# Optimization experiments

Hardware: AMD Instinct MI355X
Metric: run time of the kernel (lower is better)

## Reference

```python
import jax, jax.numpy as jnp
import numpy as np

N, D_IN, H, OUT, L = 6144, 512, 512, 256, 3
EPS = 1e-5


def setup_inputs() -> dict:
    key = jax.random.key(0)
    ks = jax.random.split(key, 32)
    inp = {}
    inp["X"] = jax.random.normal(ks[0], (N, D_IN), dtype=jnp.float32)
    inp["adj"] = jax.random.randint(ks[1], (N, N), 0, 2).astype(jnp.float32)
    inp["adj_glo"] = jax.random.randint(ks[2], (N, N), 0, 2).astype(jnp.float32)
    s = 1.0 / np.sqrt(H)
    # projection + its BN
    inp["Wp"] = jax.random.normal(ks[3], (H, D_IN), dtype=jnp.float32) / np.sqrt(D_IN)
    inp["bp"] = jnp.zeros((H,), jnp.float32)
    inp["gp"] = jnp.ones((H,), jnp.float32)
    inp["betap"] = jnp.zeros((H,), jnp.float32)
    # per-layer params; layers 0,1 output H, layer 2 outputs OUT
    outs = [H, H, OUT]
    for i in range(L):
        o = outs[i]
        k = jax.random.split(ks[4 + i], 6)
        inp[f"Wq{i}"] = jax.random.normal(k[0], (H, H), jnp.float32) * s
        inp[f"Wk{i}"] = jax.random.normal(k[1], (H, H), jnp.float32) * s
        inp[f"Wv{i}"] = jax.random.normal(k[2], (H, H), jnp.float32) * s
        inp[f"Wo{i}"] = jax.random.normal(k[3], (o, H), jnp.float32) * s
        inp[f"bo{i}"] = jnp.zeros((o,), jnp.float32)
        inp[f"g{i}"] = jnp.ones((o,), jnp.float32)
        inp[f"beta{i}"] = jnp.zeros((o,), jnp.float32)
    return inp


def _normalize_adj(a):
    # symmetric GCN normalization D^{-1/2} A D^{-1/2}
    d = a.sum(axis=1)
    dis = jnp.where(d > 0, jax.lax.rsqrt(jnp.maximum(d, 1e-12)), 0.0)
    return a * dis[:, None] * dis[None, :]


def _bn(x, g, b):
    # BatchNorm1d, training mode: batch stats, biased variance
    m = x.mean(axis=0)
    v = x.var(axis=0)
    return g * (x - m) * jax.lax.rsqrt(v + EPS) + b


def _attn(h, adj, Wq, Wk, Wv, Wo, bo):
    Q = h @ Wq.T
    K = h @ Wk.T
    V = h @ Wv.T
    scores = (Q @ K.T) / np.sqrt(H)            # [N, N]
    scores = jnp.where(adj == 0, -jnp.inf, scores)
    attn = jax.nn.softmax(scores, axis=-1)
    return (attn @ V) @ Wo.T + bo


def reference(X, adj, adj_glo, Wp, bp, gp, betap,
              Wq0, Wk0, Wv0, Wo0, bo0, g0, beta0,
              Wq1, Wk1, Wv1, Wo1, bo1, g1, beta1,
              Wq2, Wk2, Wv2, Wo2, bo2, g2, beta2):
    # embedding: normalized global adjacency aggregation + projection + BN
    h = _normalize_adj(adj_glo) @ X
    h = h @ Wp.T + bp
    h = _bn(h, gp, betap)
    embed_features = h
    layers = [
        (Wq0, Wk0, Wv0, Wo0, bo0, g0, beta0),
        (Wq1, Wk1, Wv1, Wo1, bo1, g1, beta1),
        (Wq2, Wk2, Wv2, Wo2, bo2, g2, beta2),
    ]
    for i, (Wq, Wk, Wv, Wo, bo, g, b) in enumerate(layers):
        h_s = h
        h = _attn(h, adj, Wq, Wk, Wv, Wo, bo)
        h = jax.nn.relu(_bn(h, g, b))
        if i != L - 1:
            h = h + h_s
    return h, embed_features
```

## Files before the change

### kernel.cpp

```cpp
#include <hip/hip_runtime.h>
#include <cstdint>

#define NROW 6144
#define HDIM 512
#define DOUT 256
#define NEG_INF (-__builtin_inff())

typedef _Float16 half8 __attribute__((ext_vector_type(8)));
typedef _Float16 half4v __attribute__((ext_vector_type(4)));
typedef float f32x4 __attribute__((ext_vector_type(4)));

__device__ __forceinline__ void gld_lds16(void* lds, const void* g) {
  __builtin_amdgcn_global_load_lds(
      (const __attribute__((address_space(1))) void*)g,
      (__attribute__((address_space(3))) void*)lds, 16, 0, 0);
}

__global__ __launch_bounds__(512)
void gemm256(const _Float16* __restrict__ A, int lda,
             const _Float16* __restrict__ B, int ldb,
             _Float16* __restrict__ C, int ldc, int Kc, long MN)
{
  __shared__ _Float16 As[2][256][32];
  __shared__ _Float16 Bs[2][256][32];
  const int tid = threadIdx.x;
  const int wave = tid >> 6, lane = tid & 63;
  const int wr = wave >> 2, wc = wave & 3;

  const int gx = gridDim.x, gy = gridDim.y;
  const int nwg = gx * gy * gridDim.z;
  int lin = (blockIdx.z * gy + blockIdx.y) * gx + blockIdx.x;
  int swz = (nwg % 8 == 0) ? ((lin % 8) * (nwg >> 3) + (lin >> 3)) : lin;
  const int bx = swz % gx;
  const int by = (swz / gx) % gy;
  const int bz = swz / (gx * gy);
  const int row0 = bx * 256, col0 = by * 256;
  const int kbase = bz * Kc;
  const int nt = Kc >> 5;

  const int g0 = wave * 64 + lane;
  const int g1 = g0 + 512;
  const int r0g = g0 >> 2, p0g = g0 & 3;
  const int r1g = g1 >> 2, p1g = g1 & 3;
  const size_t aoff0 = (size_t)(row0 + r0g) * lda + (p0g ^ ((r0g >> 1) & 3)) * 8;
  const size_t aoff1 = (size_t)(row0 + r1g) * lda + (p1g ^ ((r1g >> 1) & 3)) * 8;
  const size_t boff0 = (size_t)(col0 + r0g) * ldb + (p0g ^ ((r0g >> 1) & 3)) * 8;
  const size_t boff1 = (size_t)(col0 + r1g) * ldb + (p1g ^ ((r1g >> 1) & 3)) * 8;
  const int ldsh0 = (wave * 64) * 8;
  const int ldsh1 = (512 + wave * 64) * 8;

  f32x4 acc[8][4];
  const f32x4 vzero = {0.f, 0.f, 0.f, 0.f};
  #pragma unroll
  for (int f = 0; f < 8; ++f)
    #pragma unroll
    for (int j = 0; j < 4; ++j)
      acc[f][j] = vzero;

  const int fr = lane & 15, sq = lane >> 4;

  {
    const _Float16* a = A + kbase;
    const _Float16* b = B + kbase;
    gld_lds16(&As[0][0][0] + ldsh0, a + aoff0);
    gld_lds16(&As[0][0][0] + ldsh1, a + aoff1);
    gld_lds16(&Bs[0][0][0] + ldsh0, b + boff0);
    gld_lds16(&Bs[0][0][0] + ldsh1, b + boff1);
    gld_lds16(&As[1][0][0] + ldsh0, a + 32 + aoff0);
    gld_lds16(&As[1][0][0] + ldsh1, a + 32 + aoff1);
    gld_lds16(&Bs[1][0][0] + ldsh0, b + 32 + boff0);
    gld_lds16(&Bs[1][0][0] + ldsh1, b + 32 + boff1);
  }
  asm volatile("s_waitcnt vmcnt(4)" ::: "memory");
  __builtin_amdgcn_s_barrier();
  asm volatile("" ::: "memory");

  for (int t = 0; t < nt; ++t) {
    const int buf = t & 1;
    half8 bfr[4];
    #pragma unroll
    for (int j = 0; j < 4; ++j) {
      int r = wc * 64 + j * 16 + fr;
      bfr[j] = *(const half8*)&Bs[buf][r][(sq ^ ((r >> 1) & 3)) * 8];
    }
    #pragma unroll
    for (int mh = 0; mh < 2; ++mh) {
      half8 afr[4];
      #pragma unroll
      for (int i = 0; i < 4; ++i) {
        int r = wr * 128 + mh * 64 + i * 16 + fr;
        afr[i] = *(const half8*)&As[buf][r][(sq ^ ((r >> 1) & 3)) * 8];
      }
      __builtin_amdgcn_s_setprio(1);
      #pragma unroll
      for (int i = 0; i < 4; ++i)
        #pragma unroll
        for (int j = 0; j < 4; ++j)
          acc[mh * 4 + i][j] =
              __builtin_amdgcn_mfma_f32_16x16x32_f16(afr[i], bfr[j], acc[mh * 4 + i][j], 0, 0, 0);
      __builtin_amdgcn_s_setprio(0);
    }
    if (t + 1 < nt) {
      asm volatile("s_waitcnt lgkmcnt(0)" ::: "memory");
      __builtin_amdgcn_s_barrier();
      if (t + 2 < nt) {
        const _Float16* a = A + kbase + (t + 2) * 32;
        const _Float16* b = B + kbase + (t + 2) * 32;
        gld_lds16(&As[buf][0][0] + ldsh0, a + aoff0);
        gld_lds16(&As[buf][0][0] + ldsh1, a + aoff1);
        gld_lds16(&Bs[buf][0][0] + ldsh0, b + boff0);
        gld_lds16(&Bs[buf][0][0] + ldsh1, b + boff1);
        asm volatile("s_waitcnt vmcnt(4)" ::: "memory");
      } else {
        asm volatile("s_waitcnt vmcnt(0)" ::: "memory");
      }
      __builtin_amdgcn_s_barrier();
      asm volatile("" ::: "memory");
    }
  }

  _Float16* dst = C + (size_t)bz * MN;
  #pragma unroll
  for (int f = 0; f < 8; ++f)
    #pragma unroll
    for (int j = 0; j < 4; ++j)
      #pragma unroll
      for (int r = 0; r < 4; ++r) {
        int row = row0 + wr * 128 + f * 16 + sq * 4 + r;
        int col = col0 + wc * 64 + j * 16 + fr;
        dst[(size_t)row * ldc + col] = (_Float16)acc[f][j][r];
      }
}

__global__ __launch_bounds__(256)
void gemm_f16(const _Float16* __restrict__ A, int lda,
              const _Float16* __restrict__ B, int ldb,
              float* __restrict__ Cf, _Float16* __restrict__ Ch, int ldc,
              int Kc, _Float16* __restrict__ Pk, long MN)
{
  __shared__ _Float16 As[128][32];
  __shared__ _Float16 Bs[128][32];
  const int tid = threadIdx.x;
  const int wave = tid >> 6, lane = tid & 63;
  const int wr = wave >> 1, wc = wave & 1;
  const int row0 = blockIdx.x * 128, col0 = blockIdx.y * 128;
  const int kbase = blockIdx.z * Kc;

  const int sr = lane >> 2;
  const int sk = ((lane & 3) ^ ((lane >> 3) & 3)) * 8;

  f32x4 acc[4][4];
  const f32x4 vzero = {0.f, 0.f, 0.f, 0.f};
  #pragma unroll
  for (int i = 0; i < 4; ++i)
    #pragma unroll
    for (int j = 0; j < 4; ++j)
      acc[i][j] = vzero;

  const int fr = lane & 15;
  const int fk = (((lane >> 4) ^ ((fr >> 1) & 3))) * 8;

  for (int k0 = kbase; k0 < kbase + Kc; k0 += 32) {
    #pragma unroll
    for (int c = 0; c < 2; ++c) {
      int rbase = c * 64 + wave * 16;
      gld_lds16(&As[rbase][0], A + (size_t)(row0 + rbase + sr) * lda + k0 + sk);
      gld_lds16(&Bs[rbase][0], B + (size_t)(col0 + rbase + sr) * ldb + k0 + sk);
    }
    __syncthreads();
    half8 af[4], bf[4];
    #pragma unroll
    for (int i = 0; i < 4; ++i)
      af[i] = *(const half8*)&As[wr * 64 + i * 16 + fr][fk];
    #pragma unroll
    for (int j = 0; j < 4; ++j)
      bf[j] = *(const half8*)&Bs[wc * 64 + j * 16 + fr][fk];
    #pragma unroll
    for (int i = 0; i < 4; ++i)
      #pragma unroll
      for (int j = 0; j < 4; ++j)
        acc[i][j] = __builtin_amdgcn_mfma_f32_16x16x32_f16(af[i], bf[j], acc[i][j], 0, 0, 0);
    __syncthreads();
  }

  const int lr = (lane >> 4) * 4;
  const int lc = lane & 15;
  if (Pk) {
    _Float16* dst = Pk + (size_t)blockIdx.z * MN;
    #pragma unroll
    for (int i = 0; i < 4; ++i)
      #pragma unroll
      for (int j = 0; j < 4; ++j)
        #pragma unroll
        for (int r = 0; r < 4; ++r) {
          int row = row0 + wr * 64 + i * 16 + lr + r;
          int col = col0 + wc * 64 + j * 16 + lc;
          dst[(size_t)row * ldc + col] = (_Float16)acc[i][j][r];
        }
    return;
  }
  #pragma unroll
  for (int i = 0; i < 4; ++i)
    #pragma unroll
    for (int j = 0; j < 4; ++j)
      #pragma unroll
      for (int r = 0; r < 4; ++r) {
        int row = row0 + wr * 64 + i * 16 + lr + r;
        int col = col0 + wc * 64 + j * 16 + lc;
        float v = acc[i][j][r];
        if (Cf) Cf[(size_t)row * ldc + col] = v;
        if (Ch) Ch[(size_t)row * ldc + col] = (_Float16)v;
      }
}

__global__ __launch_bounds__(256)
void reduce_splitk(const _Float16* __restrict__ Pk, long MN, int S, int cshift,
                   const float* __restrict__ rowscale,
                   float* __restrict__ Yf, _Float16* __restrict__ Yh)
{
  long n4 = MN >> 2;
  for (long i = (long)blockIdx.x * 256 + threadIdx.x; i < n4; i += (long)gridDim.x * 256) {
    float s0 = 0, s1 = 0, s2 = 0, s3 = 0;
    for (int z = 0; z < S; ++z) {
      half4v p = ((const half4v*)(Pk + (size_t)z * MN))[i];
      s0 += (float)p[0]; s1 += (float)p[1]; s2 += (float)p[2]; s3 += (float)p[3];
    }
    if (rowscale) {
      float sc = rowscale[(i * 4) >> cshift];
      s0 *= sc; s1 *= sc; s2 *= sc; s3 *= sc;
    }
    if (Yf) {
      float4 o; o.x = s0; o.y = s1; o.z = s2; o.w = s3;
      ((float4*)Yf)[i] = o;
    }
    if (Yh) {
      half4v o;
      o[0] = (_Float16)s0; o[1] = (_Float16)s1; o[2] = (_Float16)s2; o[3] = (_Float16)s3;
      ((half4v*)Yh)[i] = o;
    }
  }
}

__global__ __launch_bounds__(256)
void degree_convert(const float* __restrict__ A, _Float16* __restrict__ Ah,
                    float* __restrict__ dis)
{
  const int row = blockIdx.x;
  const float* a = A + (size_t)row * NROW;
  _Float16* o = Ah + (size_t)row * NROW;
  float s = 0.f;
  #pragma unroll
  for (int it = 0; it < 6; ++it) {
    int j = it * 1024 + threadIdx.x * 4;
    float4 v = *(const float4*)&a[j];
    s += v.x + v.y + v.z + v.w;
    half4v h;
    h[0] = (_Float16)v.x; h[1] = (_Float16)v.y; h[2] = (_Float16)v.z; h[3] = (_Float16)v.w;
    *(half4v*)&o[j] = h;
  }
  #pragma unroll
  for (int off = 32; off; off >>= 1) s += __shfl_xor(s, off);
  __shared__ float red[4];
  if ((threadIdx.x & 63) == 0) red[threadIdx.x >> 6] = s;
  __syncthreads();
  if (threadIdx.x == 0) {
    float d = red[0] + red[1] + red[2] + red[3];
    dis[row] = (d > 0.f) ? rsqrtf(fmaxf(d, 1e-12f)) : 0.f;
  }
}

__global__ __launch_bounds__(192)
void build_mask(const float* __restrict__ adj, uint32_t* __restrict__ bits)
{
  const int row = blockIdx.x;
  const int w = threadIdx.x;
  const float* a = adj + (size_t)row * NROW + w * 32;
  uint32_t m = 0;
  #pragma unroll
  for (int q = 0; q < 8; ++q) {
    float4 x = *(const float4*)&a[q * 4];
    m |= (x.x != 0.f ? 1u : 0u) << (q * 4 + 0);
    m |= (x.y != 0.f ? 1u : 0u) << (q * 4 + 1);
    m |= (x.z != 0.f ? 1u : 0u) << (q * 4 + 2);
    m |= (x.w != 0.f ? 1u : 0u) << (q * 4 + 3);
  }
  bits[(size_t)row * 192 + w] = m;
}

__global__ __launch_bounds__(256)
void convert_f16(const float* __restrict__ x, _Float16* __restrict__ y, float scale, long n4)
{
  for (long i = (long)blockIdx.x * 256 + threadIdx.x; i < n4; i += (long)gridDim.x * 256) {
    float4 v = ((const float4*)x)[i];
    half4v o;
    o[0] = (_Float16)(v.x * scale);
    o[1] = (_Float16)(v.y * scale);
    o[2] = (_Float16)(v.z * scale);
    o[3] = (_Float16)(v.w * scale);
    ((half4v*)y)[i] = o;
  }
}

__global__ __launch_bounds__(256)
void transpose_scale_f16(const float* __restrict__ src, const float* __restrict__ rowscale,
                         _Float16* __restrict__ dst, int R, int C)
{
  __shared__ _Float16 tile[64][72];
  const int c0 = blockIdx.x * 64, r0 = blockIdx.y * 64;
  const int tx4 = (threadIdx.x & 15) * 4, ty = threadIdx.x >> 4;
  #pragma unroll
  for (int p = 0; p < 4; ++p) {
    int r = p * 16 + ty;
    float4 v = *(const float4*)&src[(size_t)(r0 + r) * C + c0 + tx4];
    float sc = rowscale ? rowscale[r0 + r] : 1.0f;
    tile[tx4 + 0][r] = (_Float16)(v.x * sc);
    tile[tx4 + 1][r] = (_Float16)(v.y * sc);
    tile[tx4 + 2][r] = (_Float16)(v.z * sc);
    tile[tx4 + 3][r] = (_Float16)(v.w * sc);
  }
  __syncthreads();
  #pragma unroll
  for (int p = 0; p < 4; ++p) {
    int c = p * 16 + ty;
    half4v o;
    o[0] = tile[c][tx4 + 0];
    o[1] = tile[c][tx4 + 1];
    o[2] = tile[c][tx4 + 2];
    o[3] = tile[c][tx4 + 3];
    *(half4v*)&dst[(size_t)(c0 + c) * R + r0 + tx4] = o;
  }
}

__global__ __launch_bounds__(256)
void transpose_f16(const _Float16* __restrict__ src, int ld,
                   _Float16* __restrict__ dst, int R, int C)
{
  __shared__ _Float16 tile[64][72];
  const int c0 = blockIdx.x * 64, r0 = blockIdx.y * 64;
  const int tx4 = (threadIdx.x & 15) * 4, ty = threadIdx.x >> 4;
  #pragma unroll
  for (int p = 0; p < 4; ++p) {
    int r = p * 16 + ty;
    half4v v = *(const half4v*)&src[(size_t)(r0 + r) * ld + c0 + tx4];
    tile[tx4 + 0][r] = v[0];
    tile[tx4 + 1][r] = v[1];
    tile[tx4 + 2][r] = v[2];
    tile[tx4 + 3][r] = v[3];
  }
  __syncthreads();
  #pragma unroll
  for (int p = 0; p < 4; ++p) {
    int c = p * 16 + ty;
    half4v o;
    o[0] = tile[c][tx4 + 0];
    o[1] = tile[c][tx4 + 1];
    o[2] = tile[c][tx4 + 2];
    o[3] = tile[c][tx4 + 3];
    *(half4v*)&dst[(size_t)(c0 + c) * R + r0 + tx4] = o;
  }
}

__global__ __launch_bounds__(256)
void softmax_mask16(_Float16* __restrict__ Sf, const uint32_t* __restrict__ bits,
                    float* __restrict__ linv)
{
  const int row = blockIdx.x;
  _Float16* s = Sf + (size_t)row * NROW;
  const uint32_t* b = bits + (size_t)row * 192;
  const int tid = threadIdx.x;
  float v[24];
  float m = NEG_INF;
  #pragma unroll
  for (int it = 0; it < 3; ++it) {
    int j = it * 2048 + tid * 8;
    half8 sv = *(const half8*)&s[j];
    uint32_t w = (b[j >> 5] >> (j & 31)) & 0xffu;
    #pragma unroll
    for (int e = 0; e < 8; ++e) {
      float x = ((w >> e) & 1u) ? (float)sv[e] : NEG_INF;
      v[it * 8 + e] = x;
      m = fmaxf(m, x);
    }
  }
  #pragma unroll
  for (int off = 32; off; off >>= 1) m = fmaxf(m, __shfl_xor(m, off));
  __shared__ float red[4];
  const int lane = tid & 63, wave = tid >> 6;
  if (lane == 0) red[wave] = m;
  __syncthreads();
  m = fmaxf(fmaxf(red[0], red[1]), fmaxf(red[2], red[3]));
  __syncthreads();
  float l = 0.f;
  #pragma unroll
  for (int k = 0; k < 24; ++k) {
    float e = (v[k] == NEG_INF) ? 0.f : __expf(v[k] - m);
    v[k] = e; l += e;
  }
  #pragma unroll
  for (int off = 32; off; off >>= 1) l += __shfl_xor(l, off);
  if (lane == 0) red[wave] = l;
  __syncthreads();
  l = red[0] + red[1] + red[2] + red[3];
  if (tid == 0) linv[row] = (l > 0.f) ? (1.f / l) : 0.f;
  #pragma unroll
  for (int it = 0; it < 3; ++it) {
    int j = it * 2048 + tid * 8;
    half8 o;
    #pragma unroll
    for (int e = 0; e < 8; ++e) o[e] = (_Float16)v[it * 8 + e];
    *(half8*)&s[j] = o;
  }
}

__global__ __launch_bounds__(256)
void bn_partial(const _Float16* __restrict__ X, int C,
                float* __restrict__ psum, float* __restrict__ psq)
{
  const int b = blockIdx.x;
  const int tid = threadIdx.x;
  const _Float16* x = X + (size_t)b * 128 * C;
  float s0 = 0, q0 = 0, s1 = 0, q1 = 0;
  for (int r = 0; r < 128; ++r) {
    float a = (float)x[(size_t)r * C + tid];
    s0 += a; q0 += a * a;
    if (C == 512) {
      float c2 = (float)x[(size_t)r * C + tid + 256];
      s1 += c2; q1 += c2 * c2;
    }
  }
  psum[b * C + tid] = s0; psq[b * C + tid] = q0;
  if (C == 512) { psum[b * C + tid + 256] = s1; psq[b * C + tid + 256] = q1; }
}

__global__ void bn_finalize(const float* __restrict__ psum, const float* __restrict__ psq,
                            int C, const float* __restrict__ g, const float* __restrict__ beta,
                            float* __restrict__ scale, float* __restrict__ shift)
{
  int c = threadIdx.x + blockIdx.x * blockDim.x;
  if (c >= C) return;
  float s = 0, q = 0;
  for (int b = 0; b < 48; ++b) { s += psum[b * C + c]; q += psq[b * C + c]; }
  const float invN = 1.0f / 6144.0f;
  float mean = s * invN;
  float var = q * invN - mean * mean;
  float rstd = rsqrtf(fmaxf(var, 0.f) + 1e-5f);
  float sc = g[c] * rstd;
  scale[c] = sc;
  shift[c] = beta[c] - mean * sc;
}

__global__ __launch_bounds__(256)
void bn_apply(const _Float16* __restrict__ X, const float* __restrict__ scale,
              const float* __restrict__ shift, const _Float16* __restrict__ residual,
              float* __restrict__ Yf, _Float16* __restrict__ Yh,
              int Cmask, long total, int do_relu)
{
  for (long i = (long)blockIdx.x * 256 + threadIdx.x; i < total; i += (long)gridDim.x * 256) {
    int c = (int)(i & Cmask);
    float v = (float)X[i] * scale[c] + shift[c];
    if (do_relu) v = fmaxf(v, 0.f);
    if (residual) v += (float)residual[i];
    if (Yf) Yf[i] = v;
    if (Yh) Yh[i] = (_Float16)v;
  }
}

extern "C" void kernel_launch(void* const* d_in, const int* in_sizes, int n_in,
                              void* d_out, int out_size, void* d_ws, size_t ws_size,
                              hipStream_t stream)
{
  (void)in_sizes; (void)n_in; (void)out_size; (void)ws_size;
  const float* X     = (const float*)d_in[0];
  const float* adj   = (const float*)d_in[1];
  const float* adjg  = (const float*)d_in[2];
  const float* Wp    = (const float*)d_in[3];
  const float* gp    = (const float*)d_in[5];
  const float* betap = (const float*)d_in[6];

  float* out_h     = (float*)d_out;
  float* out_embed = out_h + (size_t)NROW * DOUT;

  char* base = (char*)d_ws;
  size_t off = 0;
  auto alloc = [&](size_t bytes) -> void* {
    void* p = base + off;
    off += (bytes + 255) & ~(size_t)255;
    return p;
  };

  const long MN512 = (long)NROW * 512;

  _Float16* Ag  = (_Float16*)alloc((size_t)NROW * NROW * 2);
  _Float16* Sf  = Ag;
  uint32_t* bits = (uint32_t*)alloc((size_t)NROW * 192 * 4);
  _Float16* Pk  = (_Float16*)alloc((size_t)8 * MN512 * 2);
  _Float16* XsT = (_Float16*)alloc((size_t)HDIM * NROW * 2);
  _Float16* Yh16 = (_Float16*)alloc((size_t)NROW * HDIM * 2);
  _Float16* Wph = (_Float16*)alloc((size_t)HDIM * HDIM * 2);
  _Float16* QKVW[3];
  for (int i = 0; i < 3; ++i) QKVW[i] = (_Float16*)alloc((size_t)1536 * HDIM * 2);
  _Float16* Woh[3];
  Woh[0] = (_Float16*)alloc((size_t)512 * 512 * 2);
  Woh[1] = (_Float16*)alloc((size_t)512 * 512 * 2);
  Woh[2] = (_Float16*)alloc((size_t)256 * 512 * 2);
  _Float16* QKVh = (_Float16*)alloc((size_t)NROW * 1536 * 2);
  _Float16* VTh  = (_Float16*)alloc((size_t)HDIM * NROW * 2);
  _Float16* AVh  = (_Float16*)alloc((size_t)NROW * HDIM * 2);
  _Float16* xh   = (_Float16*)alloc((size_t)NROW * HDIM * 2);
  _Float16* hb16A = (_Float16*)alloc((size_t)NROW * HDIM * 2);
  _Float16* hb16B = (_Float16*)alloc((size_t)NROW * HDIM * 2);
  float* dis  = (float*)alloc((size_t)NROW * 4);
  float* linv = (float*)alloc((size_t)NROW * 4);
  float* psum = (float*)alloc((size_t)48 * 512 * 4);
  float* psq  = (float*)alloc((size_t)48 * 512 * 4);
  float* bnsc = (float*)alloc(512 * 4);
  float* bnsh = (float*)alloc(512 * 4);

  const float qk_scale = 0.21022410381342863f;

  degree_convert<<<NROW, 256, 0, stream>>>(adjg, Ag, dis);
  build_mask<<<NROW, 192, 0, stream>>>(adj, bits);
  transpose_scale_f16<<<dim3(8, 96), 256, 0, stream>>>(X, dis, XsT, NROW, HDIM);
  convert_f16<<<128, 256, 0, stream>>>(Wp, Wph, 1.f, 512 * 512 / 4);
  for (int i = 0; i < 3; ++i) {
    const float* Wq = (const float*)d_in[7 + i * 7 + 0];
    const float* Wk = (const float*)d_in[7 + i * 7 + 1];
    const float* Wv = (const float*)d_in[7 + i * 7 + 2];
    const float* Wo = (const float*)d_in[7 + i * 7 + 3];
    int o = (i < 2) ? 512 : 256;
    convert_f16<<<128, 256, 0, stream>>>(Wq, QKVW[i], qk_scale, 512 * 512 / 4);
    convert_f16<<<128, 256, 0, stream>>>(Wk, QKVW[i] + 512 * 512, qk_scale, 512 * 512 / 4);
    convert_f16<<<128, 256, 0, stream>>>(Wv, QKVW[i] + 2 * 512 * 512, 1.f, 512 * 512 / 4);
    convert_f16<<<128, 256, 0, stream>>>(Wo, Woh[i], 1.f, (long)o * 512 / 4);
  }

  gemm256<<<dim3(24, 2, 8), 512, 0, stream>>>(Ag, NROW, XsT, NROW, Pk, 512, 768, MN512);
  reduce_splitk<<<1536, 256, 0, stream>>>(Pk, MN512, 8, 9, dis, nullptr, Yh16);
  gemm_f16<<<dim3(48, 4), 256, 0, stream>>>(Yh16, HDIM, Wph, HDIM, nullptr, xh, HDIM,
                                            512, nullptr, 0);
  bn_partial<<<48, 256, 0, stream>>>(xh, 512, psum, psq);
  bn_finalize<<<2, 256, 0, stream>>>(psum, psq, 512, gp, betap, bnsc, bnsh);
  bn_apply<<<2048, 256, 0, stream>>>(xh, bnsc, bnsh, nullptr, out_embed, hb16A,
                                     511, MN512, 0);

  _Float16* hbuf[2] = {hb16A, hb16B};
  int cur = 0;
  for (int i = 0; i < 3; ++i) {
    int o = (i < 2) ? 512 : 256;
    const float* gl = (const float*)d_in[7 + i * 7 + 5];
    const float* bl = (const float*)d_in[7 + i * 7 + 6];
    _Float16* hin = hbuf[cur];

    gemm_f16<<<dim3(48, 12), 256, 0, stream>>>(hin, HDIM, QKVW[i], HDIM, nullptr, QKVh, 1536,
                                               512, nullptr, 0);
    transpose_f16<<<dim3(8, 96), 256, 0, stream>>>(QKVh + 1024, 1536, VTh, NROW, HDIM);
    gemm256<<<dim3(24, 24), 512, 0, stream>>>(QKVh, 1536, QKVh + 512, 1536, Sf, NROW, 512, 0);
    softmax_mask16<<<NROW, 256, 0, stream>>>(Sf, bits, linv);
    gemm256<<<dim3(24, 2, 8), 512, 0, stream>>>(Sf, NROW, VTh, NROW, Pk, 512, 768, MN512);
    reduce_splitk<<<1536, 256, 0, stream>>>(Pk, MN512, 8, 9, linv, nullptr, AVh);
    long MNo = (long)NROW * o;
    gemm_f16<<<dim3(48, o / 128, 4), 256, 0, stream>>>(AVh, HDIM, Woh[i], HDIM,
                                                       nullptr, nullptr, o, 128, Pk, MNo);
    reduce_splitk<<<1536, 256, 0, stream>>>(Pk, MNo, 4, (o == 512) ? 9 : 8, nullptr,
                                            nullptr, xh);
    bn_partial<<<48, 256, 0, stream>>>(xh, o, psum, psq);
    bn_finalize<<<2, 256, 0, stream>>>(psum, psq, o, gl, bl, bnsc, bnsh);
    if (i < 2) {
      bn_apply<<<2048, 256, 0, stream>>>(xh, bnsc, bnsh, hin, nullptr, hbuf[cur ^ 1],
                                         o - 1, (long)NROW * o, 1);
      cur ^= 1;
    } else {
      bn_apply<<<2048, 256, 0, stream>>>(xh, bnsc, bnsh, nullptr, out_h, nullptr,
                                         o - 1, (long)NROW * o, 1);
    }
  }
}
```

Measured before the change: 1.035 ms.

## Rework gemm256 into 64-wide K tiles with interleaved quadrant pipeline and split-K 16

The 256x256 GEMM kernel now stages K tiles of 64 instead of 32, with an XOR swizzle across eight 16-byte groups. Its main loop is split into quadrant-sized MFMA phases, and each phase overlaps global-to-LDS loads with LDS reads and math, separated by barriers. Launch bounds now ask for two workgroups per CU, and the N×N by N×512 aggregation GEMMs use split-K 16 instead of 8. The aim is better latency hiding and more workgroups in flight. The cost is double the LDS footprint, many more barriers, and twice the partial-sum traffic in the reduction.

```diff
diff --git a/kernel.cpp b/kernel.cpp
--- a/kernel.cpp
+++ b/kernel.cpp
@@ -10,19 +10,24 @@
 typedef _Float16 half4v __attribute__((ext_vector_type(4)));
 typedef float f32x4 __attribute__((ext_vector_type(4)));
 
+#define BARRIER() asm volatile("s_barrier" ::: "memory")
+#define LGKM0()   asm volatile("s_waitcnt lgkmcnt(0)" ::: "memory")
+#define VMCNT4()  asm volatile("s_waitcnt vmcnt(4)" ::: "memory")
+#define VMCNT0()  asm volatile("s_waitcnt vmcnt(0)" ::: "memory")
+
 __device__ __forceinline__ void gld_lds16(void* lds, const void* g) {
   __builtin_amdgcn_global_load_lds(
       (const __attribute__((address_space(1))) void*)g,
       (__attribute__((address_space(3))) void*)lds, 16, 0, 0);
 }
 
-__global__ __launch_bounds__(512)
+__global__ __launch_bounds__(512, 2)
 void gemm256(const _Float16* __restrict__ A, int lda,
              const _Float16* __restrict__ B, int ldb,
              _Float16* __restrict__ C, int ldc, int Kc, long MN)
 {
-  __shared__ _Float16 As[2][256][32];
-  __shared__ _Float16 Bs[2][256][32];
+  __shared__ _Float16 As[2][256][64];
+  __shared__ _Float16 Bs[2][256][64];
   const int tid = threadIdx.x;
   const int wave = tid >> 6, lane = tid & 63;
   const int wr = wave >> 2, wc = wave & 3;
@@ -31,24 +36,28 @@
   const int nwg = gx * gy * gridDim.z;
   int lin = (blockIdx.z * gy + blockIdx.y) * gx + blockIdx.x;
   int swz = (nwg % 8 == 0) ? ((lin % 8) * (nwg >> 3) + (lin >> 3)) : lin;
-  const int bx = swz % gx;
-  const int by = (swz / gx) % gy;
-  const int bz = swz / (gx * gy);
+  const int bx = swz % gx, by = (swz / gx) % gy, bz = swz / (gx * gy);
   const int row0 = bx * 256, col0 = by * 256;
-  const int kbase = bz * Kc;
-  const int nt = Kc >> 5;
-
-  const int g0 = wave * 64 + lane;
-  const int g1 = g0 + 512;
-  const int r0g = g0 >> 2, p0g = g0 & 3;
-  const int r1g = g1 >> 2, p1g = g1 & 3;
-  const size_t aoff0 = (size_t)(row0 + r0g) * lda + (p0g ^ ((r0g >> 1) & 3)) * 8;
-  const size_t aoff1 = (size_t)(row0 + r1g) * lda + (p1g ^ ((r1g >> 1) & 3)) * 8;
-  const size_t boff0 = (size_t)(col0 + r0g) * ldb + (p0g ^ ((r0g >> 1) & 3)) * 8;
-  const size_t boff1 = (size_t)(col0 + r1g) * ldb + (p1g ^ ((r1g >> 1) & 3)) * 8;
-  const int ldsh0 = (wave * 64) * 8;
-  const int ldsh1 = (512 + wave * 64) * 8;
-
+  const _Float16* Ab = A + (size_t)row0 * lda + (size_t)bz * Kc;
+  const _Float16* Bb = B + (size_t)col0 * ldb + (size_t)bz * Kc;
+  const int nt = Kc >> 6;
+
+  const int srow = lane >> 3;
+  const int sgr  = (lane & 7) ^ srow;
+
+  auto stageA = [&](int buf, int h, int t) {
+    const _Float16* src = Ab + (size_t)(h * 128 + wave * 8 + srow) * lda + t * 64 + sgr * 8;
+    gld_lds16(&As[buf][h * 128 + wave * 8][0], src);
+    gld_lds16(&As[buf][h * 128 + 64 + wave * 8][0], src + (size_t)64 * lda);
+  };
+  auto stageB = [&](int buf, int h, int t) {
+    const _Float16* src = Bb + (size_t)(h * 128 + wave * 8 + srow) * ldb + t * 64 + sgr * 8;
+    gld_lds16(&Bs[buf][h * 128 + wave * 8][0], src);
+    gld_lds16(&Bs[buf][h * 128 + 64 + wave * 8][0], src + (size_t)64 * ldb);
+  };
+
+  const int fr = lane & 15, sq = lane >> 4, fx = fr & 7;
+  half8 af[4][2], bLo[2][2], bHi[2][2];
   f32x4 acc[8][4];
   const f32x4 vzero = {0.f, 0.f, 0.f, 0.f};
   #pragma unroll
@@ -57,66 +66,84 @@
     for (int j = 0; j < 4; ++j)
       acc[f][j] = vzero;
 
-  const int fr = lane & 15, sq = lane >> 4;
-
-  {
-    const _Float16* a = A + kbase;
-    const _Float16* b = B + kbase;
-    gld_lds16(&As[0][0][0] + ldsh0, a + aoff0);
-    gld_lds16(&As[0][0][0] + ldsh1, a + aoff1);
-    gld_lds16(&Bs[0][0][0] + ldsh0, b + boff0);
-    gld_lds16(&Bs[0][0][0] + ldsh1, b + boff1);
-    gld_lds16(&As[1][0][0] + ldsh0, a + 32 + aoff0);
-    gld_lds16(&As[1][0][0] + ldsh1, a + 32 + aoff1);
-    gld_lds16(&Bs[1][0][0] + ldsh0, b + 32 + boff0);
-    gld_lds16(&Bs[1][0][0] + ldsh1, b + 32 + boff1);
-  }
-  asm volatile("s_waitcnt vmcnt(4)" ::: "memory");
-  __builtin_amdgcn_s_barrier();
-  asm volatile("" ::: "memory");
-
-  for (int t = 0; t < nt; ++t) {
-    const int buf = t & 1;
-    half8 bfr[4];
-    #pragma unroll
-    for (int j = 0; j < 4; ++j) {
-      int r = wc * 64 + j * 16 + fr;
-      bfr[j] = *(const half8*)&Bs[buf][r][(sq ^ ((r >> 1) & 3)) * 8];
-    }
-    #pragma unroll
-    for (int mh = 0; mh < 2; ++mh) {
-      half8 afr[4];
-      #pragma unroll
-      for (int i = 0; i < 4; ++i) {
-        int r = wr * 128 + mh * 64 + i * 16 + fr;
-        afr[i] = *(const half8*)&As[buf][r][(sq ^ ((r >> 1) & 3)) * 8];
-      }
-      __builtin_amdgcn_s_setprio(1);
-      #pragma unroll
-      for (int i = 0; i < 4; ++i)
+  auto dsA = [&](int buf, int mh) {
+    #pragma unroll
+    for (int i = 0; i < 4; ++i)
+      #pragma unroll
+      for (int ks = 0; ks < 2; ++ks)
+        af[i][ks] = *(const half8*)&As[buf][wr * 128 + mh * 64 + i * 16 + fr]
+                                          [((ks * 4 + sq) ^ fx) * 8];
+  };
+  auto dsBlo = [&](int buf) {
+    #pragma unroll
+    for (int jj = 0; jj < 2; ++jj)
+      #pragma unroll
+      for (int ks = 0; ks < 2; ++ks)
+        bLo[jj][ks] = *(const half8*)&Bs[buf][wc * 64 + jj * 16 + fr]
+                                            [((ks * 4 + sq) ^ fx) * 8];
+  };
+  auto dsBhi = [&](int buf) {
+    #pragma unroll
+    for (int jj = 0; jj < 2; ++jj)
+      #pragma unroll
+      for (int ks = 0; ks < 2; ++ks)
+        bHi[jj][ks] = *(const half8*)&Bs[buf][wc * 64 + 32 + jj * 16 + fr]
+                                            [((ks * 4 + sq) ^ fx) * 8];
+  };
+  auto mQlo = [&](int fb) {
+    __builtin_amdgcn_s_setprio(1);
+    #pragma unroll
+    for (int i = 0; i < 4; ++i)
+      #pragma unroll
+      for (int jj = 0; jj < 2; ++jj)
         #pragma unroll
-        for (int j = 0; j < 4; ++j)
-          acc[mh * 4 + i][j] =
-              __builtin_amdgcn_mfma_f32_16x16x32_f16(afr[i], bfr[j], acc[mh * 4 + i][j], 0, 0, 0);
-      __builtin_amdgcn_s_setprio(0);
-    }
-    if (t + 1 < nt) {
-      asm volatile("s_waitcnt lgkmcnt(0)" ::: "memory");
-      __builtin_amdgcn_s_barrier();
-      if (t + 2 < nt) {
-        const _Float16* a = A + kbase + (t + 2) * 32;
-        const _Float16* b = B + kbase + (t + 2) * 32;
-        gld_lds16(&As[buf][0][0] + ldsh0, a + aoff0);
-        gld_lds16(&As[buf][0][0] + ldsh1, a + aoff1);
-        gld_lds16(&Bs[buf][0][0] + ldsh0, b + boff0);
-        gld_lds16(&Bs[buf][0][0] + ldsh1, b + boff1);
-        asm volatile("s_waitcnt vmcnt(4)" ::: "memory");
-      } else {
-        asm volatile("s_waitcnt vmcnt(0)" ::: "memory");
-      }
-      __builtin_amdgcn_s_barrier();
-      asm volatile("" ::: "memory");
-    }
+        for (int ks = 0; ks < 2; ++ks)
+          acc[fb + i][jj] = __builtin_amdgcn_mfma_f32_16x16x32_f16(
+              af[i][ks], bLo[jj][ks], acc[fb + i][jj], 0, 0, 0);
+    __builtin_amdgcn_s_setprio(0);
+  };
+  auto mQhi = [&](int fb) {
+    __builtin_amdgcn_s_setprio(1);
+    #pragma unroll
+    for (int i = 0; i < 4; ++i)
+      #pragma unroll
+      for (int jj = 0; jj < 2; ++jj)
+        #pragma unroll
+        for (int ks = 0; ks < 2; ++ks)
+          acc[fb + i][2 + jj] = __builtin_amdgcn_mfma_f32_16x16x32_f16(
+              af[i][ks], bHi[jj][ks], acc[fb + i][2 + jj], 0, 0, 0);
+    __builtin_amdgcn_s_setprio(0);
+  };
+
+  stageA(0, 0, 0); stageA(0, 1, 0); stageB(0, 0, 0); stageB(0, 1, 0);
+  stageB(1, 0, 1); stageB(1, 1, 1);
+  VMCNT4();
+  BARRIER();
+
+  for (int T = 0; T < nt; T += 2) {
+    const bool pipe = (T + 2 < nt);
+    dsA(0, 0); dsBlo(0);
+    stageA(1, 0, T + 1);
+    BARRIER(); LGKM0(); mQlo(0); BARRIER();
+    dsBhi(0);
+    stageA(1, 1, T + 1);
+    BARRIER(); LGKM0(); mQhi(0); BARRIER();
+    dsA(0, 1);
+    if (pipe) stageB(0, 0, T + 2);
+    BARRIER(); LGKM0(); mQhi(4); BARRIER();
+    if (pipe) { stageB(0, 1, T + 2); VMCNT4(); } else { VMCNT0(); }
+    BARRIER(); mQlo(4); BARRIER();
+    dsA(1, 0); dsBlo(1);
+    if (pipe) stageA(0, 0, T + 2);
+    BARRIER(); LGKM0(); mQlo(0); BARRIER();
+    dsBhi(1);
+    if (pipe) stageA(0, 1, T + 2);
+    BARRIER(); LGKM0(); mQhi(0); BARRIER();
+    dsA(1, 1);
+    if (pipe) stageB(1, 0, T + 3);
+    BARRIER(); LGKM0(); mQhi(4); BARRIER();
+    if (pipe) { stageB(1, 1, T + 3); VMCNT4(); } else { VMCNT0(); }
+    BARRIER(); mQlo(4); BARRIER();
   }
 
   _Float16* dst = C + (size_t)bz * MN;
@@ -493,7 +520,7 @@
   _Float16* Ag  = (_Float16*)alloc((size_t)NROW * NROW * 2);
   _Float16* Sf  = Ag;
   uint32_t* bits = (uint32_t*)alloc((size_t)NROW * 192 * 4);
-  _Float16* Pk  = (_Float16*)alloc((size_t)8 * MN512 * 2);
+  _Float16* Pk  = (_Float16*)alloc((size_t)16 * MN512 * 2);
   _Float16* XsT = (_Float16*)alloc((size_t)HDIM * NROW * 2);
   _Float16* Yh16 = (_Float16*)alloc((size_t)NROW * HDIM * 2);
   _Float16* Wph = (_Float16*)alloc((size_t)HDIM * HDIM * 2);
@@ -534,8 +561,8 @@
     convert_f16<<<128, 256, 0, stream>>>(Wo, Woh[i], 1.f, (long)o * 512 / 4);
   }
 
-  gemm256<<<dim3(24, 2, 8), 512, 0, stream>>>(Ag, NROW, XsT, NROW, Pk, 512, 768, MN512);
-  reduce_splitk<<<1536, 256, 0, stream>>>(Pk, MN512, 8, 9, dis, nullptr, Yh16);
+  gemm256<<<dim3(24, 2, 16), 512, 0, stream>>>(Ag, NROW, XsT, NROW, Pk, 512, 384, MN512);
+  reduce_splitk<<<1536, 256, 0, stream>>>(Pk, MN512, 16, 9, dis, nullptr, Yh16);
   gemm_f16<<<dim3(48, 4), 256, 0, stream>>>(Yh16, HDIM, Wph, HDIM, nullptr, xh, HDIM,
                                             512, nullptr, 0);
   bn_partial<<<48, 256, 0, stream>>>(xh, 512, psum, psq);
@@ -556,8 +583,8 @@
     transpose_f16<<<dim3(8, 96), 256, 0, stream>>>(QKVh + 1024, 1536, VTh, NROW, HDIM);
     gemm256<<<dim3(24, 24), 512, 0, stream>>>(QKVh, 1536, QKVh + 512, 1536, Sf, NROW, 512, 0);
     softmax_mask16<<<NROW, 256, 0, stream>>>(Sf, bits, linv);
-    gemm256<<<dim3(24, 2, 8), 512, 0, stream>>>(Sf, NROW, VTh, NROW, Pk, 512, 768, MN512);
-    reduce_splitk<<<1536, 256, 0, stream>>>(Pk, MN512, 8, 9, linv, nullptr, AVh);
+    gemm256<<<dim3(24, 2, 16), 512, 0, stream>>>(Sf, NROW, VTh, NROW, Pk, 512, 384, MN512);
+    reduce_splitk<<<1536, 256, 0, stream>>>(Pk, MN512, 16, 9, linv, nullptr, AVh);
     long MNo = (long)NROW * o;
     gemm_f16<<<dim3(48, o / 128, 4), 256, 0, stream>>>(AVh, HDIM, Woh[i], HDIM,
                                                        nullptr, nullptr, o, 128, Pk, MNo);
```

Result: faster. 997.8 us (-3.6%).
